# Performance work log

Hardware: AMD Instinct MI355X
Metric: run time of the kernel (lower is better)

The kernel has to match this reference:

```python
import jax, jax.numpy as jnp
import numpy as np

NUM_GRAPHS = 1024


def setup_inputs() -> dict:
    key = jax.random.key(0)
    k1, k2, k3, k4 = jax.random.split(key, 4)
    N, IN, OUT = 500000, 128, 128
    x = jax.random.normal(k1, (N, IN), dtype=jnp.float32)
    batch_id = jnp.sort(jax.random.randint(k2, (N,), 0, NUM_GRAPHS))
    # torch Linear: weight [out_features, in_features_total]
    W = jax.random.normal(k3, (OUT, 2 * IN), dtype=jnp.float32) * (1.0 / np.sqrt(2 * IN))
    b = jax.random.normal(k4, (OUT,), dtype=jnp.float32) * 0.01
    return {"x": x, "batch_id": batch_id, "W": W, "b": b}


def reference(x, batch_id, W, b):
    # global_mean_pool: segment-mean of x over batch_id -> [G, IN]
    sums = jax.ops.segment_sum(x, batch_id, num_segments=NUM_GRAPHS)
    counts = jax.ops.segment_sum(jnp.ones((x.shape[0],), dtype=x.dtype), batch_id,
                                 num_segments=NUM_GRAPHS)
    mean = sums / jnp.maximum(counts, 1.0)[:, None]  # [G, IN]
    # gather per-graph context back to each node, concat, linear
    g_per_node = mean[batch_id]                      # [N, IN]
    inp = jnp.concatenate([x, g_per_node], axis=-1)  # [N, 2*IN]
    return inp @ W.T + b                             # [N, OUT]
```

## Files before the change

### kernel.cpp

```cpp
#include <hip/hip_runtime.h>


#define G_NUM 1024
#define IN_F 128
#define OUT_F 128

typedef __attribute__((ext_vector_type(8))) short short8;
typedef __attribute__((ext_vector_type(4))) float f32x4;
typedef __attribute__((ext_vector_type(4))) unsigned short us4;

static __device__ __forceinline__ unsigned short f2bf(float f) {
    union { float f; unsigned u; } v; v.f = f;
    unsigned u = v.u;
    return (unsigned short)((u + 0x7FFFu + ((u >> 16) & 1u)) >> 16);
}

static __device__ __forceinline__ us4 pack4(float4 a) {
    us4 o;
    o[0] = f2bf(a.x); o[1] = f2bf(a.y); o[2] = f2bf(a.z); o[3] = f2bf(a.w);
    return o;
}

static __device__ __forceinline__ short8 pack8(float4 a, float4 b) {
    short8 o;
    o[0] = (short)f2bf(a.x); o[1] = (short)f2bf(a.y);
    o[2] = (short)f2bf(a.z); o[3] = (short)f2bf(a.w);
    o[4] = (short)f2bf(b.x); o[5] = (short)f2bf(b.y);
    o[6] = (short)f2bf(b.z); o[7] = (short)f2bf(b.w);
    return o;
}

template <bool WXB>
__global__ __launch_bounds__(256) void k_pass1(
        const float* __restrict__ x, const int* __restrict__ bid,
        const float* __restrict__ W, const float* __restrict__ b,
        float* __restrict__ ctx, unsigned short* __restrict__ W1b,
        unsigned short* __restrict__ xb, int N) {
    int g = blockIdx.x;
    int tid = threadIdx.x;

    if (tid < 16) {
        int i = (g << 4) + tid;
        W1b[i] = f2bf(W[(i >> 7) * 256 + (i & 127)]);
    }

    int lo = 0, hi = N;
    while (lo < hi) { int m = (lo + hi) >> 1; if (bid[m] < g) lo = m + 1; else hi = m; }
    int start = lo;
    int lo2 = start, hi2 = N;
    while (lo2 < hi2) { int m = (lo2 + hi2) >> 1; if (bid[m] < g + 1) lo2 = m + 1; else hi2 = m; }
    int end = lo2;
    int cnt = end - start;

    __shared__ float4 red[8][32];
    __shared__ float ms[IN_F];

    int c4 = tid & 31;
    int rg = tid >> 5;
    float4 s0 = make_float4(0.f, 0.f, 0.f, 0.f);
    float4 s1 = s0, s2 = s0, s3 = s0;

    int r = start + rg;
    for (; r + 24 < end; r += 32) {
        float4 a = *(const float4*)(x + (size_t)(r     ) * IN_F + c4 * 4);
        float4 c = *(const float4*)(x + (size_t)(r +  8) * IN_F + c4 * 4);
        float4 d = *(const float4*)(x + (size_t)(r + 16) * IN_F + c4 * 4);
        float4 e = *(const float4*)(x + (size_t)(r + 24) * IN_F + c4 * 4);
        if (WXB) {
            *(us4*)(xb + (size_t)(r     ) * IN_F + c4 * 4) = pack4(a);
            *(us4*)(xb + (size_t)(r +  8) * IN_F + c4 * 4) = pack4(c);
            *(us4*)(xb + (size_t)(r + 16) * IN_F + c4 * 4) = pack4(d);
            *(us4*)(xb + (size_t)(r + 24) * IN_F + c4 * 4) = pack4(e);
        }
        s0.x += a.x; s0.y += a.y; s0.z += a.z; s0.w += a.w;
        s1.x += c.x; s1.y += c.y; s1.z += c.z; s1.w += c.w;
        s2.x += d.x; s2.y += d.y; s2.z += d.z; s2.w += d.w;
        s3.x += e.x; s3.y += e.y; s3.z += e.z; s3.w += e.w;
    }
    for (; r < end; r += 8) {
        float4 a = *(const float4*)(x + (size_t)r * IN_F + c4 * 4);
        if (WXB) *(us4*)(xb + (size_t)r * IN_F + c4 * 4) = pack4(a);
        s0.x += a.x; s0.y += a.y; s0.z += a.z; s0.w += a.w;
    }
    s0.x += s1.x + s2.x + s3.x;
    s0.y += s1.y + s2.y + s3.y;
    s0.z += s1.z + s2.z + s3.z;
    s0.w += s1.w + s2.w + s3.w;

    red[rg][c4] = s0;
    __syncthreads();
    if (tid < 32) {
        float4 t = red[0][tid];
        #pragma unroll
        for (int i = 1; i < 8; ++i) {
            float4 v = red[i][tid];
            t.x += v.x; t.y += v.y; t.z += v.z; t.w += v.w;
        }
        float inv = 1.0f / (float)(cnt > 0 ? cnt : 1);
        ms[tid * 4 + 0] = t.x * inv;
        ms[tid * 4 + 1] = t.y * inv;
        ms[tid * 4 + 2] = t.z * inv;
        ms[tid * 4 + 3] = t.w * inv;
    }
    __syncthreads();
    if (tid < OUT_F) {
        int o = tid;
        float acc = b[o];
        const float* w2 = W + o * 256 + 128;
        #pragma unroll 8
        for (int k = 0; k < IN_F; ++k) acc += ms[k] * w2[k];
        ctx[g * OUT_F + o] = acc;
    }
}

__global__ __launch_bounds__(256, 3) void k_gemm_bf(
        const unsigned short* __restrict__ xb, const int* __restrict__ bid,
        const unsigned short* __restrict__ W1b, const float* __restrict__ ctx,
        float* __restrict__ out, int N) {
    int tid = threadIdx.x;
    int row0 = blockIdx.x * 128;
    int lane = tid & 63, wave = tid >> 6;
    int l16 = lane & 15, quad = lane >> 4;
    int wrow = wave * 32;

    f32x4 acc[2][8];
    #pragma unroll
    for (int mt = 0; mt < 2; ++mt)
        #pragma unroll
        for (int ot = 0; ot < 8; ++ot)
            acc[mt][ot] = (f32x4){0.f, 0.f, 0.f, 0.f};

    #pragma unroll
    for (int kt = 0; kt < 4; ++kt) {
        short8 af[2];
        #pragma unroll
        for (int mt = 0; mt < 2; ++mt) {
            int rrow = row0 + wrow + mt * 16 + l16;
            short8 v = (short8){0, 0, 0, 0, 0, 0, 0, 0};
            if (rrow < N)
                v = *(const short8*)(xb + (size_t)rrow * IN_F + kt * 32 + quad * 8);
            af[mt] = v;
        }
        #pragma unroll
        for (int ot = 0; ot < 8; ++ot) {
            short8 bf = *(const short8*)(W1b + (ot * 16 + l16) * IN_F + kt * 32 + quad * 8);
            acc[0][ot] = __builtin_amdgcn_mfma_f32_16x16x32_bf16(af[0], bf, acc[0][ot], 0, 0, 0);
            acc[1][ot] = __builtin_amdgcn_mfma_f32_16x16x32_bf16(af[1], bf, acc[1][ot], 0, 0, 0);
        }
    }

    int lastrow = row0 + 127 < N ? row0 + 127 : N - 1;
    int b_lo = bid[row0], b_hi = bid[lastrow];
    if (b_lo == b_hi) {
        float cv[8];
        #pragma unroll
        for (int ot = 0; ot < 8; ++ot)
            cv[ot] = ctx[b_lo * OUT_F + ot * 16 + l16];
        #pragma unroll
        for (int mt = 0; mt < 2; ++mt) {
            #pragma unroll
            for (int r4 = 0; r4 < 4; ++r4) {
                int row = row0 + wrow + mt * 16 + quad * 4 + r4;
                if (row < N) {
                    #pragma unroll
                    for (int ot = 0; ot < 8; ++ot)
                        out[(size_t)row * OUT_F + ot * 16 + l16] =
                            acc[mt][ot][r4] + cv[ot];
                }
            }
        }
    } else {
        #pragma unroll
        for (int mt = 0; mt < 2; ++mt) {
            #pragma unroll
            for (int r4 = 0; r4 < 4; ++r4) {
                int row = row0 + wrow + mt * 16 + quad * 4 + r4;
                if (row < N) {
                    int cb = bid[row] * OUT_F;
                    #pragma unroll
                    for (int ot = 0; ot < 8; ++ot)
                        out[(size_t)row * OUT_F + ot * 16 + l16] =
                            acc[mt][ot][r4] + ctx[cb + ot * 16 + l16];
                }
            }
        }
    }
}

__global__ __launch_bounds__(256, 2) void k_gemm_f32(
        const float* __restrict__ x, const int* __restrict__ bid,
        const unsigned short* __restrict__ W1b, const float* __restrict__ ctx,
        float* __restrict__ out, int N) {
    int tid = threadIdx.x;
    int row0 = blockIdx.x * 128;
    int lane = tid & 63, wave = tid >> 6;
    int l16 = lane & 15, quad = lane >> 4;
    int wrow = (wave & 1) * 64;
    int wcol = (wave >> 1) * 64;

    f32x4 acc[4][4];
    #pragma unroll
    for (int mt = 0; mt < 4; ++mt)
        #pragma unroll
        for (int ot = 0; ot < 4; ++ot)
            acc[mt][ot] = (f32x4){0.f, 0.f, 0.f, 0.f};

    #pragma unroll
    for (int kt = 0; kt < 4; ++kt) {
        short8 bf[4];
        #pragma unroll
        for (int ot = 0; ot < 4; ++ot)
            bf[ot] = *(const short8*)(W1b + (wcol + ot * 16 + l16) * IN_F + kt * 32 + quad * 8);
        short8 af[4];
        #pragma unroll
        for (int mt = 0; mt < 4; ++mt) {
            int r = row0 + wrow + mt * 16 + l16;
            float4 v0 = make_float4(0.f, 0.f, 0.f, 0.f), v1 = v0;
            if (r < N) {
                const float* p = x + (size_t)r * IN_F + kt * 32 + quad * 8;
                v0 = *(const float4*)p;
                v1 = *(const float4*)(p + 4);
            }
            af[mt] = pack8(v0, v1);
        }
        #pragma unroll
        for (int mt = 0; mt < 4; ++mt)
            #pragma unroll
            for (int ot = 0; ot < 4; ++ot)
                acc[mt][ot] = __builtin_amdgcn_mfma_f32_16x16x32_bf16(
                    af[mt], bf[ot], acc[mt][ot], 0, 0, 0);
    }

    int lastrow = row0 + 127 < N ? row0 + 127 : N - 1;
    int b_lo = bid[row0], b_hi = bid[lastrow];
    if (b_lo == b_hi) {
        float cv[4];
        #pragma unroll
        for (int ot = 0; ot < 4; ++ot)
            cv[ot] = ctx[b_lo * OUT_F + wcol + ot * 16 + l16];
        #pragma unroll
        for (int mt = 0; mt < 4; ++mt) {
            #pragma unroll
            for (int r4 = 0; r4 < 4; ++r4) {
                int row = row0 + wrow + mt * 16 + quad * 4 + r4;
                if (row < N) {
                    #pragma unroll
                    for (int ot = 0; ot < 4; ++ot)
                        out[(size_t)row * OUT_F + wcol + ot * 16 + l16] =
                            acc[mt][ot][r4] + cv[ot];
                }
            }
        }
    } else {
        #pragma unroll
        for (int mt = 0; mt < 4; ++mt) {
            #pragma unroll
            for (int r4 = 0; r4 < 4; ++r4) {
                int row = row0 + wrow + mt * 16 + quad * 4 + r4;
                if (row < N) {
                    int cb = bid[row] * OUT_F;
                    #pragma unroll
                    for (int ot = 0; ot < 4; ++ot)
                        out[(size_t)row * OUT_F + wcol + ot * 16 + l16] =
                            acc[mt][ot][r4] + ctx[cb + wcol + ot * 16 + l16];
                }
            }
        }
    }
}

extern "C" void kernel_launch(void* const* d_in, const int* in_sizes, int n_in,
                              void* d_out, int out_size, void* d_ws, size_t ws_size,
                              hipStream_t stream) {
    const float* x  = (const float*)d_in[0];
    const int* bid  = (const int*)d_in[1];
    const float* W  = (const float*)d_in[2];
    const float* b  = (const float*)d_in[3];
    float* out      = (float*)d_out;
    int N = in_sizes[1];

    size_t ctx_bytes = (size_t)G_NUM * OUT_F * sizeof(float);
    size_t w1b_bytes = (size_t)OUT_F * IN_F * sizeof(unsigned short);
    float* ctx = (float*)d_ws;
    unsigned short* W1b = (unsigned short*)((char*)d_ws + ctx_bytes);
    unsigned short* xb  = (unsigned short*)((char*)d_ws + ctx_bytes + w1b_bytes);
    size_t need = ctx_bytes + w1b_bytes + (size_t)N * IN_F * sizeof(unsigned short);

    if (ws_size >= need) {
        k_pass1<true><<<G_NUM, 256, 0, stream>>>(x, bid, W, b, ctx, W1b, xb, N);
        k_gemm_bf<<<(N + 127) / 128, 256, 0, stream>>>(xb, bid, W1b, ctx, out, N);
    } else {
        k_pass1<false><<<G_NUM, 256, 0, stream>>>(x, bid, W, b, ctx, W1b, nullptr, N);
        k_gemm_f32<<<(N + 127) / 128, 256, 0, stream>>>(x, bid, W1b, ctx, out, N);
    }
}
```

Measured before the change: 541.0 us.

## Fuse segment-mean pooling and GEMM into one per-graph kernel with LDS-staged x

Adds a single kernel with one block per graph. Each block reduces its rows for the mean, stages up to 616 rows of x as bf16 in a swizzled LDS buffer, computes the per-graph context vector, then runs the MFMA GEMM from LDS and writes the output. The goal is to read x from HBM once, instead of once in pass1 and again (or a bf16 copy) in the GEMM, and to drop the second launch. In exchange it uses about 160KB of LDS, so one block per CU, and only 1024 blocks. The fallback path no longer checks the workspace size before writing the bf16 copy, which could overflow a small workspace.

```diff
diff --git a/kernel.cpp b/kernel.cpp
--- a/kernel.cpp
+++ b/kernel.cpp
@@ -4,6 +4,8 @@
 #define G_NUM 1024
 #define IN_F 128
 #define OUT_F 128
+#define CAP 616
+#define SMEM_BYTES (5120 + CAP * 256)
 
 typedef __attribute__((ext_vector_type(8))) short short8;
 typedef __attribute__((ext_vector_type(4))) float f32x4;
@@ -28,6 +30,149 @@
     o[4] = (short)f2bf(b.x); o[5] = (short)f2bf(b.y);
     o[6] = (short)f2bf(b.z); o[7] = (short)f2bf(b.w);
     return o;
+}
+
+__global__ __launch_bounds__(256, 1) void k_fused(
+        const float* __restrict__ x, const int* __restrict__ bid,
+        const float* __restrict__ W, const float* __restrict__ b,
+        float* __restrict__ out, int N) {
+    extern __shared__ char smem[];
+    float4 (*red)[32] = (float4 (*)[32])(smem);
+    float* ms   = (float*)(smem + 4096);
+    float* ctxs = (float*)(smem + 4608);
+    char* xs    = smem + 5120;
+
+    int g = blockIdx.x;
+    int tid = threadIdx.x;
+
+    int lo = 0, hi = N;
+    while (lo < hi) { int m = (lo + hi) >> 1; if (bid[m] < g) lo = m + 1; else hi = m; }
+    int start = lo;
+    int lo2 = start, hi2 = N;
+    while (lo2 < hi2) { int m = (lo2 + hi2) >> 1; if (bid[m] < g + 1) lo2 = m + 1; else hi2 = m; }
+    int end = lo2;
+    int cnt = end - start;
+
+    int c4 = tid & 31;
+    int rg = tid >> 5;
+    int uu = c4 >> 1;
+    int hb = (c4 & 1) * 8;
+    float4 s0 = make_float4(0.f, 0.f, 0.f, 0.f);
+    float4 s1 = s0, s2 = s0, s3 = s0;
+
+    int r = start + rg;
+    for (; r + 24 < end; r += 32) {
+        const float* p0 = x + (size_t)r * IN_F + c4 * 4;
+        float4 a = *(const float4*)(p0);
+        float4 c = *(const float4*)(p0 +  8 * IN_F);
+        float4 d = *(const float4*)(p0 + 16 * IN_F);
+        float4 e = *(const float4*)(p0 + 24 * IN_F);
+        int lr = r - start;
+        int sw = ((uu ^ (lr & 7)) << 4) + hb;
+        if (lr      < CAP) *(us4*)(xs + (size_t)(lr     ) * 256 + sw) = pack4(a);
+        if (lr +  8 < CAP) *(us4*)(xs + (size_t)(lr +  8) * 256 + sw) = pack4(c);
+        if (lr + 16 < CAP) *(us4*)(xs + (size_t)(lr + 16) * 256 + sw) = pack4(d);
+        if (lr + 24 < CAP) *(us4*)(xs + (size_t)(lr + 24) * 256 + sw) = pack4(e);
+        s0.x += a.x; s0.y += a.y; s0.z += a.z; s0.w += a.w;
+        s1.x += c.x; s1.y += c.y; s1.z += c.z; s1.w += c.w;
+        s2.x += d.x; s2.y += d.y; s2.z += d.z; s2.w += d.w;
+        s3.x += e.x; s3.y += e.y; s3.z += e.z; s3.w += e.w;
+    }
+    for (; r < end; r += 8) {
+        float4 a = *(const float4*)(x + (size_t)r * IN_F + c4 * 4);
+        int lr = r - start;
+        if (lr < CAP) *(us4*)(xs + (size_t)lr * 256 + ((uu ^ (lr & 7)) << 4) + hb) = pack4(a);
+        s0.x += a.x; s0.y += a.y; s0.z += a.z; s0.w += a.w;
+    }
+    s0.x += s1.x + s2.x + s3.x;
+    s0.y += s1.y + s2.y + s3.y;
+    s0.z += s1.z + s2.z + s3.z;
+    s0.w += s1.w + s2.w + s3.w;
+
+    red[rg][c4] = s0;
+    __syncthreads();
+
+    int lane = tid & 63, wave = tid >> 6;
+    int l16 = lane & 15, quad = lane >> 4;
+
+    short8 bw[4][8];
+    #pragma unroll
+    for (int kt = 0; kt < 4; ++kt)
+        #pragma unroll
+        for (int ot = 0; ot < 8; ++ot) {
+            const float* wp = W + (size_t)(ot * 16 + l16) * 256 + kt * 32 + quad * 8;
+            bw[kt][ot] = pack8(*(const float4*)wp, *(const float4*)(wp + 4));
+        }
+
+    if (tid < 32) {
+        float4 t = red[0][tid];
+        #pragma unroll
+        for (int i = 1; i < 8; ++i) {
+            float4 v = red[i][tid];
+            t.x += v.x; t.y += v.y; t.z += v.z; t.w += v.w;
+        }
+        float inv = 1.0f / (float)(cnt > 0 ? cnt : 1);
+        ms[tid * 4 + 0] = t.x * inv;
+        ms[tid * 4 + 1] = t.y * inv;
+        ms[tid * 4 + 2] = t.z * inv;
+        ms[tid * 4 + 3] = t.w * inv;
+    }
+    __syncthreads();
+    if (tid < OUT_F) {
+        float acc = b[tid];
+        const float* w2 = W + (size_t)tid * 256 + 128;
+        #pragma unroll 8
+        for (int k = 0; k < IN_F; ++k) acc += ms[k] * w2[k];
+        ctxs[tid] = acc;
+    }
+    __syncthreads();
+
+    float cv[8];
+    #pragma unroll
+    for (int ot = 0; ot < 8; ++ot) cv[ot] = ctxs[ot * 16 + l16];
+
+    int ntiles = (cnt + 15) >> 4;
+    for (int t = wave; t < ntiles; t += 4) {
+        int lr = t * 16 + l16;
+        short8 af[4];
+        if (lr < cnt && lr < CAP) {
+            const char* rp = xs + (size_t)lr * 256;
+            int swb = lr & 7;
+            #pragma unroll
+            for (int kt = 0; kt < 4; ++kt)
+                af[kt] = *(const short8*)(rp + (((kt * 4 + quad) ^ swb) << 4));
+        } else if (lr < cnt) {
+            const float* p = x + (size_t)(start + lr) * IN_F;
+            #pragma unroll
+            for (int kt = 0; kt < 4; ++kt)
+                af[kt] = pack8(*(const float4*)(p + kt * 32 + quad * 8),
+                               *(const float4*)(p + kt * 32 + quad * 8 + 4));
+        } else {
+            #pragma unroll
+            for (int kt = 0; kt < 4; ++kt) af[kt] = (short8){0, 0, 0, 0, 0, 0, 0, 0};
+        }
+
+        f32x4 acc[8];
+        #pragma unroll
+        for (int ot = 0; ot < 8; ++ot) acc[ot] = (f32x4){0.f, 0.f, 0.f, 0.f};
+        #pragma unroll
+        for (int kt = 0; kt < 4; ++kt)
+            #pragma unroll
+            for (int ot = 0; ot < 8; ++ot)
+                acc[ot] = __builtin_amdgcn_mfma_f32_16x16x32_bf16(
+                    af[kt], bw[kt][ot], acc[ot], 0, 0, 0);
+
+        #pragma unroll
+        for (int r4 = 0; r4 < 4; ++r4) {
+            int rl = t * 16 + quad * 4 + r4;
+            if (rl < cnt) {
+                float* po = out + (size_t)(start + rl) * OUT_F;
+                #pragma unroll
+                for (int ot = 0; ot < 8; ++ot)
+                    po[ot * 16 + l16] = acc[ot][r4] + cv[ot];
+            }
+        }
+    }
 }
 
 template <bool WXB>
@@ -187,88 +332,6 @@
     }
 }
 
-__global__ __launch_bounds__(256, 2) void k_gemm_f32(
-        const float* __restrict__ x, const int* __restrict__ bid,
-        const unsigned short* __restrict__ W1b, const float* __restrict__ ctx,
-        float* __restrict__ out, int N) {
-    int tid = threadIdx.x;
-    int row0 = blockIdx.x * 128;
-    int lane = tid & 63, wave = tid >> 6;
-    int l16 = lane & 15, quad = lane >> 4;
-    int wrow = (wave & 1) * 64;
-    int wcol = (wave >> 1) * 64;
-
-    f32x4 acc[4][4];
-    #pragma unroll
-    for (int mt = 0; mt < 4; ++mt)
-        #pragma unroll
-        for (int ot = 0; ot < 4; ++ot)
-            acc[mt][ot] = (f32x4){0.f, 0.f, 0.f, 0.f};
-
-    #pragma unroll
-    for (int kt = 0; kt < 4; ++kt) {
-        short8 bf[4];
-        #pragma unroll
-        for (int ot = 0; ot < 4; ++ot)
-            bf[ot] = *(const short8*)(W1b + (wcol + ot * 16 + l16) * IN_F + kt * 32 + quad * 8);
-        short8 af[4];
-        #pragma unroll
-        for (int mt = 0; mt < 4; ++mt) {
-            int r = row0 + wrow + mt * 16 + l16;
-            float4 v0 = make_float4(0.f, 0.f, 0.f, 0.f), v1 = v0;
-            if (r < N) {
-                const float* p = x + (size_t)r * IN_F + kt * 32 + quad * 8;
-                v0 = *(const float4*)p;
-                v1 = *(const float4*)(p + 4);
-            }
-            af[mt] = pack8(v0, v1);
-        }
-        #pragma unroll
-        for (int mt = 0; mt < 4; ++mt)
-            #pragma unroll
-            for (int ot = 0; ot < 4; ++ot)
-                acc[mt][ot] = __builtin_amdgcn_mfma_f32_16x16x32_bf16(
-                    af[mt], bf[ot], acc[mt][ot], 0, 0, 0);
-    }
-
-    int lastrow = row0 + 127 < N ? row0 + 127 : N - 1;
-    int b_lo = bid[row0], b_hi = bid[lastrow];
-    if (b_lo == b_hi) {
-        float cv[4];
-        #pragma unroll
-        for (int ot = 0; ot < 4; ++ot)
-            cv[ot] = ctx[b_lo * OUT_F + wcol + ot * 16 + l16];
-        #pragma unroll
-        for (int mt = 0; mt < 4; ++mt) {
-            #pragma unroll
-            for (int r4 = 0; r4 < 4; ++r4) {
-                int row = row0 + wrow + mt * 16 + quad * 4 + r4;
-                if (row < N) {
-                    #pragma unroll
-                    for (int ot = 0; ot < 4; ++ot)
-                        out[(size_t)row * OUT_F + wcol + ot * 16 + l16] =
-                            acc[mt][ot][r4] + cv[ot];
-                }
-            }
-        }
-    } else {
-        #pragma unroll
-        for (int mt = 0; mt < 4; ++mt) {
-            #pragma unroll
-            for (int r4 = 0; r4 < 4; ++r4) {
-                int row = row0 + wrow + mt * 16 + quad * 4 + r4;
-                if (row < N) {
-                    int cb = bid[row] * OUT_F;
-                    #pragma unroll
-                    for (int ot = 0; ot < 4; ++ot)
-                        out[(size_t)row * OUT_F + wcol + ot * 16 + l16] =
-                            acc[mt][ot][r4] + ctx[cb + wcol + ot * 16 + l16];
-                }
-            }
-        }
-    }
-}
-
 extern "C" void kernel_launch(void* const* d_in, const int* in_sizes, int n_in,
                               void* d_out, int out_size, void* d_ws, size_t ws_size,
                               hipStream_t stream) {
@@ -279,18 +342,25 @@
     float* out      = (float*)d_out;
     int N = in_sizes[1];
 
+    static int fused_ok = -1;
+    if (fused_ok < 0) {
+        fused_ok = (hipFuncSetAttribute(
+                        reinterpret_cast<const void*>(&k_fused),
+                        hipFuncAttributeMaxDynamicSharedMemorySize,
+                        SMEM_BYTES) == hipSuccess) ? 1 : 0;
+    }
+
+    if (fused_ok) {
+        k_fused<<<G_NUM, 256, SMEM_BYTES, stream>>>(x, bid, W, b, out, N);
+        return;
+    }
+
     size_t ctx_bytes = (size_t)G_NUM * OUT_F * sizeof(float);
     size_t w1b_bytes = (size_t)OUT_F * IN_F * sizeof(unsigned short);
     float* ctx = (float*)d_ws;
     unsigned short* W1b = (unsigned short*)((char*)d_ws + ctx_bytes);
     unsigned short* xb  = (unsigned short*)((char*)d_ws + ctx_bytes + w1b_bytes);
-    size_t need = ctx_bytes + w1b_bytes + (size_t)N * IN_F * sizeof(unsigned short);
-
-    if (ws_size >= need) {
-        k_pass1<true><<<G_NUM, 256, 0, stream>>>(x, bid, W, b, ctx, W1b, xb, N);
-        k_gemm_bf<<<(N + 127) / 128, 256, 0, stream>>>(xb, bid, W1b, ctx, out, N);
-    } else {
-        k_pass1<false><<<G_NUM, 256, 0, stream>>>(x, bid, W, b, ctx, W1b, nullptr, N);
-        k_gemm_f32<<<(N + 127) / 128, 256, 0, stream>>>(x, bid, W1b, ctx, out, N);
-    }
-}
+
+    k_pass1<true><<<G_NUM, 256, 0, stream>>>(x, bid, W, b, ctx, W1b, xb, N);
+    k_gemm_bf<<<(N + 127) / 128, 256, 0, stream>>>(xb, bid, W1b, ctx, out, N);
+}
```

New measurement: 511.5 us. -5.4%, faster.
